# Performance work log

Measured on AMD Instinct MI355X. Metric: run time of the kernel, lower is better.

## Reference

```python
import jax, jax.numpy as jnp
import numpy as np

PI = np.float32(np.pi)
CNOT = jnp.array([[1,0,0,0],[0,1,0,0],[0,0,0,1],[0,0,1,0]], dtype=jnp.complex64)


def _u3(t, p, l):
    c, s = jnp.cos(t / 2), jnp.sin(t / 2)
    return jnp.stack([
        jnp.stack([c + 0j, -jnp.exp(1j * l) * s]),
        jnp.stack([jnp.exp(1j * p) * s, jnp.exp(1j * (p + l)) * c]),
    ]).astype(jnp.complex64)


def _ry(t):
    c, s = jnp.cos(t / 2), jnp.sin(t / 2)
    return jnp.stack([jnp.stack([c, -s]), jnp.stack([s, c])]).astype(jnp.complex64)


def _rz(t):
    z = jnp.zeros((), jnp.complex64)
    return jnp.stack([
        jnp.stack([jnp.exp(-1j * t / 2).astype(jnp.complex64), z]),
        jnp.stack([z, jnp.exp(1j * t / 2).astype(jnp.complex64)]),
    ]).astype(jnp.complex64)


def _apply1(psi, G, w):
    # psi: [N,2,2,2,2]; uniform single-qubit gate G [2,2] on wire w
    psi = jnp.moveaxis(psi, 1 + w, -1)
    psi = jnp.einsum('ij,nabcj->nabci', G, psi)
    return jnp.moveaxis(psi, -1, 1 + w)


def _apply1_batch(psi, G, w):
    # per-sample gate G [N,2,2]
    psi = jnp.moveaxis(psi, 1 + w, -1)
    psi = jnp.einsum('nij,nabcj->nabci', G, psi)
    return jnp.moveaxis(psi, -1, 1 + w)


def _apply2(psi, G, a, b):
    # two-qubit gate G [4,4] on wires (a,b)
    psi = jnp.moveaxis(psi, (1 + a, 1 + b), (-2, -1))
    psi = psi.reshape(psi.shape[:-2] + (4,))
    psi = jnp.einsum('ij,nabj->nabi', G, psi)
    psi = psi.reshape(psi.shape[:-1] + (2, 2))
    return jnp.moveaxis(psi, (-2, -1), (1 + a, 1 + b))


def _su4(psi, u3s, angs, a, b):
    # u3s: [4,3] = (w0, w1, w5, w6); angs: [3] = (w2, w3, w4)
    psi = _apply1(psi, _u3(u3s[0, 0], u3s[0, 1], u3s[0, 2]), a)
    psi = _apply1(psi, _u3(u3s[1, 0], u3s[1, 1], u3s[1, 2]), b)
    psi = _apply2(psi, CNOT, a, b)
    psi = _apply1(psi, _ry(angs[0]), a)
    psi = _apply1(psi, _rz(angs[1]), b)
    psi = _apply2(psi, CNOT, b, a)
    psi = _apply1(psi, _ry(angs[2]), a)
    psi = _apply2(psi, CNOT, a, b)
    psi = _apply1(psi, _u3(u3s[2, 0], u3s[2, 1], u3s[2, 2]), a)
    psi = _apply1(psi, _u3(u3s[3, 0], u3s[3, 1], u3s[3, 2]), b)
    return psi


def _circuit(angles, qw_u3, qw_ang):
    # angles: [N,4]; returns PauliZ expvals [N,4]
    N = angles.shape[0]
    psi = jnp.zeros((N, 2, 2, 2, 2), jnp.complex64).at[:, 0, 0, 0, 0].set(1.0)
    for w in range(4):  # AngleEmbedding: RY(angle) on each wire, per-sample
        c, s = jnp.cos(angles[:, w] / 2), jnp.sin(angles[:, w] / 2)
        G = jnp.stack([jnp.stack([c, -s], -1), jnp.stack([s, c], -1)], -2).astype(jnp.complex64)
        psi = _apply1_batch(psi, G, w)
    pairs = [(0, 1), (1, 2), (2, 3), (3, 0)]
    for layer in range(2):
        u3s = qw_u3[4 * layer:4 * layer + 4]
        angs = qw_ang[3 * layer:3 * layer + 3]
        for (a, b) in pairs:
            psi = _su4(psi, u3s, angs, a, b)
    p = psi.real ** 2 + psi.imag ** 2  # [N,2,2,2,2]
    z = jnp.array([1.0, -1.0], p.dtype)
    evs = [jnp.sum(p * z.reshape([1] + [2 if i == w else 1 for i in range(4)]), axis=(1, 2, 3, 4)) for w in range(4)]
    return jnp.stack(evs, -1)


def _conv(x, w, b):
    y = jax.lax.conv_general_dilated(x, w, (1, 1), 'SAME', dimension_numbers=('NCHW', 'OIHW', 'NCHW'))
    return y + b[None, :, None, None]


def _maxpool2(x):
    return jax.lax.reduce_window(x, -jnp.inf, jax.lax.max, (1, 1, 2, 2), (1, 1, 2, 2), 'VALID')


def setup_inputs() -> dict:
    key = jax.random.key(0)
    ks = jax.random.split(key, 20)
    n = jax.random.normal
    return {
        'x': n(ks[0], (1024, 3, 32, 32), jnp.float32),
        'conv1_w': n(ks[1], (64, 3, 3, 3), jnp.float32) * 0.1,
        'conv1_b': n(ks[2], (64,), jnp.float32) * 0.1,
        'conv2_w': n(ks[3], (16, 64, 3, 3), jnp.float32) * 0.05,
        'conv2_b': n(ks[4], (16,), jnp.float32) * 0.1,
        'conv3_w': n(ks[5], (4, 16, 3, 3), jnp.float32) * 0.1,
        'conv3_b': n(ks[6], (4,), jnp.float32) * 0.1,
        'qw_u3': jax.random.uniform(ks[7], (8, 3), jnp.float32, 0.0, 2 * np.pi),
        'qw_ang': jax.random.uniform(ks[8], (6,), jnp.float32, 0.0, 2 * np.pi),
        'fc1a_w': n(ks[9], (64, 256), jnp.float32) * 0.06,
        'fc1a_b': n(ks[10], (64,), jnp.float32) * 0.1,
        'fc1b_w': n(ks[11], (128, 64), jnp.float32) * 0.1,
        'fc1b_b': n(ks[12], (128,), jnp.float32) * 0.1,
        'fc2a_w': n(ks[13], (64, 128), jnp.float32) * 0.1,
        'fc2a_b': n(ks[14], (64,), jnp.float32) * 0.1,
        'fc2b_w': n(ks[15], (10, 64), jnp.float32) * 0.1,
        'fc2b_b': n(ks[16], (10,), jnp.float32) * 0.1,
    }


def reference(x, conv1_w, conv1_b, conv2_w, conv2_b, conv3_w, conv3_b,
              qw_u3, qw_ang, fc1a_w, fc1a_b, fc1b_w, fc1b_b,
              fc2a_w, fc2a_b, fc2b_w, fc2b_b):
    h = _maxpool2(jax.nn.relu(_conv(x, conv1_w, conv1_b)))      # [B,64,16,16]
    h = _maxpool2(jax.nn.relu(_conv(h, conv2_w, conv2_b)))      # [B,16,8,8]
    h = jax.nn.leaky_relu(_conv(h, conv3_w, conv3_b), 0.01)     # [B,4,8,8]
    B, C, H, W = h.shape
    # 1x1 patches in (h, w, c) order, matching torch unfold+permute
    patches = jnp.transpose(h, (0, 2, 3, 1)).reshape(B * H * W, C)
    ang = jax.nn.sigmoid(patches) * PI
    q = _circuit(ang, qw_u3, qw_ang)            # [B*64, 4]
    q = q.reshape(B, H * W * 4)                 # [B, 256]
    h1 = jax.nn.relu(q @ fc1a_w.T + fc1a_b)
    h1 = h1 @ fc1b_w.T + fc1b_b
    h2 = jax.nn.relu(h1 @ fc2a_w.T + fc2a_b)
    return h2 @ fc2b_w.T + fc2b_b               # [B, 10]
```

## Files before the change

kernel.cpp:

```cpp
#include <hip/hip_runtime.h>
#include <math.h>

#define PI_F 3.14159265358979323846f

typedef _Float16 half2_t __attribute__((ext_vector_type(2)));
typedef _Float16 f16x8 __attribute__((ext_vector_type(8)));
typedef float f32x4v __attribute__((ext_vector_type(4)));

__device__ __forceinline__ unsigned packh2(float lo, float hi) {
  unsigned short l = __builtin_bit_cast(unsigned short, (_Float16)lo);
  unsigned short h = __builtin_bit_cast(unsigned short, (_Float16)hi);
  return (unsigned)l | ((unsigned)h << 16);
}

__device__ __forceinline__ unsigned pk16(_Float16 a, _Float16 b) {
  unsigned short ua = __builtin_bit_cast(unsigned short, a);
  unsigned short ub = __builtin_bit_cast(unsigned short, b);
  return (unsigned)ua | ((unsigned)ub << 16);
}

struct c2 { float x, y; };
__device__ __forceinline__ c2 cmul(c2 a, c2 b){ return c2{a.x*b.x - a.y*b.y, a.x*b.y + a.y*b.x}; }
__device__ __forceinline__ c2 cadd(c2 a, c2 b){ return c2{a.x+b.x, a.y+b.y}; }

__device__ __forceinline__ void rot2(c2 &a, c2 &b, c2 g00, c2 g01, c2 g10, c2 g11) {
  c2 na = cadd(cmul(g00,a), cmul(g01,b));
  c2 nb = cadd(cmul(g10,a), cmul(g11,b));
  a = na; b = nb;
}

__device__ __forceinline__ void mk_u3(float th, float ph, float la,
                                      c2 &g00, c2 &g01, c2 &g10, c2 &g11) {
  float ch = cosf(0.5f*th), sh = sinf(0.5f*th);
  float cl = cosf(la), sl = sinf(la);
  float cp = cosf(ph), sp = sinf(ph);
  float cpl = cp*cl - sp*sl, spl = sp*cl + cp*sl;
  g00 = c2{ch, 0.f};
  g01 = c2{-cl*sh, -sl*sh};
  g10 = c2{cp*sh, sp*sh};
  g11 = c2{cpl*ch, spl*ch};
}

template<int MA, int MB>
__device__ __forceinline__ void apply2q(c2 psi[16], const c2 M[16]) {
#pragma unroll
  for (int r = 0; r < 16; ++r) {
    if (r & (MA | MB)) continue;
    c2 a = psi[r], b = psi[r|MB], c = psi[r|MA], d = psi[r|MA|MB];
    psi[r]        = cadd(cadd(cmul(M[0],a),  cmul(M[1],b)),  cadd(cmul(M[2],c),  cmul(M[3],d)));
    psi[r|MB]     = cadd(cadd(cmul(M[4],a),  cmul(M[5],b)),  cadd(cmul(M[6],c),  cmul(M[7],d)));
    psi[r|MA]     = cadd(cadd(cmul(M[8],a),  cmul(M[9],b)),  cadd(cmul(M[10],c), cmul(M[11],d)));
    psi[r|MA|MB]  = cadd(cadd(cmul(M[12],a), cmul(M[13],b)), cadd(cmul(M[14],c), cmul(M[15],d)));
  }
}

__global__ __launch_bounds__(256) void k_setup(const float* __restrict__ w1a, const float* __restrict__ w1b,
                                               const float* __restrict__ w2a, const float* __restrict__ w2b,
                                               const float* __restrict__ c2w,
                                               const float* __restrict__ c1w, const float* __restrict__ c1b,
                                               const float* __restrict__ qw_u3,
                                               const float* __restrict__ qw_ang,
                                               float* __restrict__ wt, float* __restrict__ A) {
  __shared__ c2 SU[2][16];
  __shared__ float Ur[16*17], Ui[16*17];
  int t = threadIdx.x;
  if (blockIdx.x == 167) {
    if (t < 8) {
      int L = t >> 2, col = t & 3;
      c2 s[4];
#pragma unroll
      for (int i = 0; i < 4; ++i) s[i] = c2{(i==col)?1.f:0.f, 0.f};
      const float* u = qw_u3 + 12*L;
      const float* g = qw_ang + 3*L;
      c2 g00,g01,g10,g11;
      mk_u3(u[0],u[1],u[2], g00,g01,g10,g11);
      rot2(s[0],s[2], g00,g01,g10,g11); rot2(s[1],s[3], g00,g01,g10,g11);
      mk_u3(u[3],u[4],u[5], g00,g01,g10,g11);
      rot2(s[0],s[1], g00,g01,g10,g11); rot2(s[2],s[3], g00,g01,g10,g11);
      { c2 tmp = s[2]; s[2] = s[3]; s[3] = tmp; }
      { float c = cosf(0.5f*g[0]), sn = sinf(0.5f*g[0]);
        c2 r00{c,0.f}, r01{-sn,0.f}, r10{sn,0.f}, r11{c,0.f};
        rot2(s[0],s[2], r00,r01,r10,r11); rot2(s[1],s[3], r00,r01,r10,r11); }
      { float c = cosf(0.5f*g[1]), sn = sinf(0.5f*g[1]);
        c2 e0{c,-sn}, e1{c,sn};
        s[0]=cmul(s[0],e0); s[1]=cmul(s[1],e1); s[2]=cmul(s[2],e0); s[3]=cmul(s[3],e1); }
      { c2 tmp = s[1]; s[1] = s[3]; s[3] = tmp; }
      { float c = cosf(0.5f*g[2]), sn = sinf(0.5f*g[2]);
        c2 r00{c,0.f}, r01{-sn,0.f}, r10{sn,0.f}, r11{c,0.f};
        rot2(s[0],s[2], r00,r01,r10,r11); rot2(s[1],s[3], r00,r01,r10,r11); }
      { c2 tmp = s[2]; s[2] = s[3]; s[3] = tmp; }
      mk_u3(u[6],u[7],u[8], g00,g01,g10,g11);
      rot2(s[0],s[2], g00,g01,g10,g11); rot2(s[1],s[3], g00,g01,g10,g11);
      mk_u3(u[9],u[10],u[11], g00,g01,g10,g11);
      rot2(s[0],s[1], g00,g01,g10,g11); rot2(s[2],s[3], g00,g01,g10,g11);
#pragma unroll
      for (int k = 0; k < 4; ++k) SU[L][k*4 + col] = s[k];
    }
    __syncthreads();
    if (t < 16) {
      c2 psi[16];
#pragma unroll
      for (int i = 0; i < 16; ++i) psi[i] = c2{(i==t)?1.f:0.f, 0.f};
#pragma unroll
      for (int l = 0; l < 2; ++l) {
        c2 M[16];
#pragma unroll
        for (int k = 0; k < 16; ++k) M[k] = SU[l][k];
        apply2q<8,4>(psi, M);
        apply2q<4,2>(psi, M);
        apply2q<2,1>(psi, M);
        apply2q<1,8>(psi, M);
      }
#pragma unroll
      for (int k = 0; k < 16; ++k) { Ur[k*17+t] = psi[k].x; Ui[k*17+t] = psi[k].y; }
    }
    __syncthreads();
    {
      int i = t >> 4, j = t & 15;
      float a0=0.f,a1=0.f,a2=0.f,a3=0.f;
#pragma unroll
      for (int k = 0; k < 16; ++k) {
        float pr = Ur[k*17+i]*Ur[k*17+j] + Ui[k*17+i]*Ui[k*17+j];
        a0 += ((k>>3)&1) ? -pr : pr;
        a1 += ((k>>2)&1) ? -pr : pr;
        a2 += ((k>>1)&1) ? -pr : pr;
        a3 += ( k     &1) ? -pr : pr;
      }
      A[0*256 + t] = a0; A[1*256 + t] = a1; A[2*256 + t] = a2; A[3*256 + t] = a3;
    }
    return;
  }
  int id = blockIdx.x*256 + t;
  if (id < 16384) { int j = id >> 6, o = id & 63;  wt[id] = w1a[o*256 + j]; return; }
  int id1 = id - 16384;
  if (id1 < 8192)  { int j = id1 >> 7, o = id1 & 127; wt[16384 + id1] = w1b[o*64 + j]; return; }
  int id2 = id1 - 8192;
  if (id2 < 8192)  { int j = id2 >> 6, o = id2 & 63;  wt[24576 + id2] = w2a[o*128 + j]; return; }
  int id3 = id2 - 8192;
  if (id3 < 640)   { int j = id3 / 10, o = id3 % 10;  wt[32768 + id3] = w2b[o*64 + j]; return; }
  int id4 = id3 - 640;
  if (id4 < 4608) {
    int s = id4 >> 8, rem = id4 & 255, l = rem >> 2, r = rem & 3;
    int tap = s >> 1, h = s & 1;
    int oc = l & 15, j = l >> 4;
    int icl = 16*h + 4*j + r;
    float lo = c2w[oc*576 + icl*9 + tap];
    float hi = c2w[oc*576 + (icl+32)*9 + tap];
    ((unsigned*)wt)[33408 + id4] = packh2(lo, hi);
    return;
  }
  int id5 = id4 - 4608;
  if (id5 < 1024) {
    int nt = id5 >> 8, rem = id5 & 255, l = rem >> 2, r = rem & 3;
    int oc = nt*16 + (l & 15), j = l >> 4;
    int k0 = 8*j + 2*r;
    float lo = (k0     < 27) ? c1w[oc*27 + k0]     : 0.f;
    float hi = (k0 + 1 < 27) ? c1w[oc*27 + k0 + 1] : 0.f;
    ((unsigned*)wt)[38016 + id5] = packh2(lo, hi);
  }
}

__global__ __launch_bounds__(512, 4) void k_conv12(
    const float* __restrict__ x,
    const uint4* __restrict__ B1g, const float* __restrict__ b1,
    const uint4* __restrict__ B2g, const float* __restrict__ b2,
    float* __restrict__ h2) {
  __shared__ _Float16 xs[3468];
  __shared__ unsigned hsp[11664];
  int b = blockIdx.x, t = threadIdx.x;
  int l = t & 63, w = t >> 6;
  int m = l & 15, j = l >> 4;
  uint4 Bf1[4];
#pragma unroll
  for (int nt = 0; nt < 4; ++nt) Bf1[nt] = B1g[nt*64 + l];
  int offs[8];
#pragma unroll
  for (int q = 0; q < 8; ++q) {
    int kk = 8*j + q;
    int kc = (kk < 27) ? kk : 0;
    int c = kc / 9, rem = kc - 9*c, wr = rem / 3, cc = rem - 3*wr;
    offs[q] = c*1156 + wr*34 + cc;
  }
  {
    unsigned* xz = (unsigned*)xs;
    for (int i = t; i < 1734; i += 512) xz[i] = 0u;
    uint4 z = make_uint4(0u,0u,0u,0u);
    uint4* hz = (uint4*)hsp;
    for (int i = t; i < 2916; i += 512) hz[i] = z;
  }
  __syncthreads();
  for (int i = t; i < 3072; i += 512) {
    int c = i >> 10, rem = i & 1023, gy = rem >> 5, gx = rem & 31;
    xs[c*1156 + (gy+1)*34 + gx + 1] = (_Float16)x[(size_t)b*3072 + i];
  }
  __syncthreads();
#pragma unroll
  for (int h = 0; h < 2; ++h) {
    f32x4v acc[2][2][4];
#pragma unroll
    for (int rr = 0; rr < 2; ++rr)
#pragma unroll
      for (int xh = 0; xh < 2; ++xh)
#pragma unroll
        for (int nt = 0; nt < 4; ++nt)
          acc[rr][xh][nt] = f32x4v{0.f, 0.f, 0.f, 0.f};
#pragma unroll
    for (int rr = 0; rr < 2; ++rr)
#pragma unroll
      for (int xh = 0; xh < 2; ++xh) {
        int base = (16*h + 2*w + rr)*34 + 16*xh + m;
        _Float16 v[8];
#pragma unroll
        for (int q = 0; q < 8; ++q) v[q] = xs[offs[q] + base];
        uint4 Au = make_uint4(pk16(v[0], v[1]), pk16(v[2], v[3]),
                              pk16(v[4], v[5]), pk16(v[6], v[7]));
        f16x8 Av = __builtin_bit_cast(f16x8, Au);
#pragma unroll
        for (int nt = 0; nt < 4; ++nt)
          acc[rr][xh][nt] = __builtin_amdgcn_mfma_f32_16x16x32_f16(
              Av, __builtin_bit_cast(f16x8, Bf1[nt]), acc[rr][xh][nt], 0, 0, 0);
      }
    {
      int pyg = 8*h + w;
#pragma unroll
      for (int ntp = 0; ntp < 2; ++ntp) {
        float bza = b1[ntp*16 + m];
        float bzb = b1[(ntp+2)*16 + m];
#pragma unroll
        for (int xh = 0; xh < 2; ++xh)
#pragma unroll
          for (int pv = 0; pv < 2; ++pv) {
            f32x4v aL0 = acc[0][xh][ntp],   aL1 = acc[1][xh][ntp];
            f32x4v aH0 = acc[0][xh][ntp+2], aH1 = acc[1][xh][ntp+2];
            float mlo = fmaxf(fmaxf(aL0[2*pv], aL0[2*pv+1]), fmaxf(aL1[2*pv], aL1[2*pv+1]));
            float mhi = fmaxf(fmaxf(aH0[2*pv], aH0[2*pv+1]), fmaxf(aH1[2*pv], aH1[2*pv+1]));
            int px = 8*xh + 2*j + pv;
            hsp[((pyg+1)*18 + px + 1)*36 + ntp*16 + m] =
                packh2(fmaxf(mlo + bza, 0.f), fmaxf(mhi + bzb, 0.f));
          }
      }
    }
  }
  __syncthreads();
  float bz2 = b2[m];
  f32x4v a2[2];
  a2[0] = f32x4v{bz2, bz2, bz2, bz2};
  a2[1] = f32x4v{bz2, bz2, bz2, bz2};
  uint4 bnx = B2g[l];
#pragma unroll
  for (int s = 0; s < 18; ++s) {
    f16x8 Bv = __builtin_bit_cast(f16x8, bnx);
    if (s < 17) bnx = B2g[(s+1)*64 + l];
    const int tap = s >> 1, hh = s & 1;
    const int dy = tap / 3, dx = tap % 3;
#pragma unroll
    for (int tt = 0; tt < 2; ++tt) {
      int y = 2*w + tt;
      f16x8 Av = __builtin_bit_cast(f16x8,
          *(const uint4*)(hsp + ((y+dy)*18 + m + dx)*36 + 16*hh + 4*j));
      a2[tt] = __builtin_amdgcn_mfma_f32_16x16x32_f16(Av, Bv, a2[tt], 0, 0, 0);
    }
  }
  float* outb = h2 + (size_t)b*1024 + m*64;
#pragma unroll
  for (int vp = 0; vp < 2; ++vp) {
    float mm = fmaxf(fmaxf(a2[0][2*vp], a2[0][2*vp+1]),
                     fmaxf(a2[1][2*vp], a2[1][2*vp+1]));
    outb[w*8 + 2*j + vp] = fmaxf(mm, 0.f);
  }
}

__global__ __launch_bounds__(256) void k_tail(const float* __restrict__ h2, const float* __restrict__ w,
                                              const float* __restrict__ bias, const float* __restrict__ Ag,
                                              const float* __restrict__ wt,
                                              const float* __restrict__ b1a, const float* __restrict__ b1b,
                                              const float* __restrict__ b2a, const float* __restrict__ b2b,
                                              float* __restrict__ out) {
  __shared__ float h3s[1600];
  __shared__ float As[1024];
  __shared__ float c3s[4][64];
  __shared__ float qs[256];
  __shared__ float red[256];
  __shared__ float h1s[64];
  __shared__ float hbv[128];
  __shared__ float h3v[64];
  int b = blockIdx.x, t = threadIdx.x;
#pragma unroll
  for (int k = 0; k < 4; ++k) As[k*256 + t] = Ag[k*256 + t];
  for (int i = t; i < 1600; i += 256) h3s[i] = 0.f;
  __syncthreads();
  {
    const float4* src = (const float4*)(h2 + (size_t)b*1024);
    float4 v = src[t];
    int e = 4*t;
    int ic = e >> 6, iy = (e >> 3) & 7, ix = e & 7;
    float* d = &h3s[ic*100 + (iy+1)*10 + ix + 1];
    d[0]=v.x; d[1]=v.y; d[2]=v.z; d[3]=v.w;
  }
  __syncthreads();
  {
    int oc = t >> 6, pos = t & 63;
    int y = pos >> 3, xo = pos & 7;
    float acc = bias[oc];
    const float* wp = w + oc*144;
    for (int ic = 0; ic < 16; ++ic) {
#pragma unroll
      for (int ky = 0; ky < 3; ++ky)
#pragma unroll
        for (int kx = 0; kx < 3; ++kx)
          acc = fmaf(wp[ic*9 + ky*3 + kx], h3s[ic*100 + (y+ky)*10 + (xo+kx)], acc);
    }
    c3s[oc][pos] = acc;
  }
  __syncthreads();
  {
    int p = t & 63, w4 = t >> 6;
    float v0[2], v1[2], v2[2], v3[2];
#pragma unroll
    for (int o = 0; o < 4; ++o) {
      float v = c3s[o][p];
      float lv = v > 0.f ? v : 0.01f*v;
      float sg = 1.f/(1.f + expf(-lv));
      float sv, cv;
      __sincosf(sg * (0.5f*PI_F), &sv, &cv);
      float* dst = (o==0)?v0:(o==1)?v1:(o==2)?v2:v3;
      dst[0] = cv; dst[1] = sv;
    }
    float pv[16];
#pragma unroll
    for (int i = 0; i < 16; ++i)
      pv[i] = v0[(i>>3)&1] * v1[(i>>2)&1] * v2[(i>>1)&1] * v3[i&1];
    const float4* Aw = (const float4*)(As + w4*256);
    float a = 0.f;
#pragma unroll
    for (int i = 0; i < 16; ++i) {
      float d = 0.f;
#pragma unroll
      for (int j4 = 0; j4 < 4; ++j4) {
        float4 av = Aw[i*4 + j4];
        d = fmaf(av.x, pv[j4*4+0], d);
        d = fmaf(av.y, pv[j4*4+1], d);
        d = fmaf(av.z, pv[j4*4+2], d);
        d = fmaf(av.w, pv[j4*4+3], d);
      }
      a = fmaf(pv[i], d, a);
    }
    qs[p*4 + w4] = a;
  }
  __syncthreads();
  const float* WT1a = wt;
  const float* WT1b = wt + 16384;
  const float* WT2a = wt + 24576;
  const float* WT2b = wt + 32768;
  {
    int o = t & 63, seg = t >> 6;
    float acc = 0.f;
    const float* wp = WT1a + seg*64*64 + o;
    const float* qp = qs + seg*64;
    for (int jj = 0; jj < 64; ++jj) acc = fmaf(wp[jj*64], qp[jj], acc);
    red[seg*64 + o] = acc;
  }
  __syncthreads();
  if (t < 64) {
    float s = red[t] + red[64+t] + red[128+t] + red[192+t] + b1a[t];
    h1s[t] = fmaxf(s, 0.f);
  }
  __syncthreads();
  if (t < 128) {
    float acc = b1b[t];
    for (int jj = 0; jj < 64; ++jj) acc = fmaf(WT1b[jj*128 + t], h1s[jj], acc);
    hbv[t] = acc;
  }
  __syncthreads();
  {
    int o = t & 63, seg = t >> 6;
    float acc = 0.f;
    const float* wp = WT2a + seg*32*64 + o;
    const float* hp = hbv + seg*32;
    for (int jj = 0; jj < 32; ++jj) acc = fmaf(wp[jj*64], hp[jj], acc);
    red[seg*64 + o] = acc;
  }
  __syncthreads();
  if (t < 64) {
    float s = red[t] + red[64+t] + red[128+t] + red[192+t] + b2a[t];
    h3v[t] = fmaxf(s, 0.f);
  }
  __syncthreads();
  if (t < 10) {
    float o = b2b[t];
    for (int jj = 0; jj < 64; ++jj) o = fmaf(WT2b[jj*10 + t], h3v[jj], o);
    out[(size_t)b*10 + t] = o;
  }
}

extern "C" void kernel_launch(void* const* d_in, const int* in_sizes, int n_in,
                              void* d_out, int out_size, void* d_ws, size_t ws_size,
                              hipStream_t stream) {
  const float* x       = (const float*)d_in[0];
  const float* conv1_w = (const float*)d_in[1];
  const float* conv1_b = (const float*)d_in[2];
  const float* conv2_w = (const float*)d_in[3];
  const float* conv2_b = (const float*)d_in[4];
  const float* conv3_w = (const float*)d_in[5];
  const float* conv3_b = (const float*)d_in[6];
  const float* qw_u3   = (const float*)d_in[7];
  const float* qw_ang  = (const float*)d_in[8];
  const float* fc1a_w  = (const float*)d_in[9];
  const float* fc1a_b  = (const float*)d_in[10];
  const float* fc1b_w  = (const float*)d_in[11];
  const float* fc1b_b  = (const float*)d_in[12];
  const float* fc2a_w  = (const float*)d_in[13];
  const float* fc2a_b  = (const float*)d_in[14];
  const float* fc2b_w  = (const float*)d_in[15];
  const float* fc2b_b  = (const float*)d_in[16];
  float* out = (float*)d_out;

  float* ws  = (float*)d_ws;
  float* A   = ws;
  float* WT  = ws + 1024;
  const uint4* BG  = (const uint4*)((const unsigned*)WT + 33408);
  const uint4* B1G = (const uint4*)((const unsigned*)WT + 38016);
  float* h2  = ws + 17083008;

  k_setup <<<168,  256, 0, stream>>>(fc1a_w, fc1b_w, fc2a_w, fc2b_w, conv2_w, conv1_w, conv1_b,
                                     qw_u3, qw_ang, WT, A);
  k_conv12<<<1024, 512, 0, stream>>>(x, B1G, conv1_b, BG, conv2_b, h2);
  k_tail  <<<1024, 256, 0, stream>>>(h2, conv3_w, conv3_b, A, WT,
                                     fc1a_b, fc1b_b, fc2a_b, fc2b_b, out);
}
```

Measured before the change: 45.87 us.

## Process two images per tail block and prefetch conv1 input before zeroing

The tail kernel now handles two batch images per block, halving the grid. This amortizes the shared-memory load of the quantum matrix and the per-block weight traffic, and uses idle threads in the small FC stages. Separately, conv12 issues its global input loads into registers before the shared-memory zeroing and barrier, so load latency overlaps with that setup. The cost is more shared memory and more serial work per tail block, with only half as many blocks to spread across CUs.

```diff
diff --git a/kernel.cpp b/kernel.cpp
--- a/kernel.cpp
+++ b/kernel.cpp
@@ -170,6 +170,9 @@
   int b = blockIdx.x, t = threadIdx.x;
   int l = t & 63, w = t >> 6;
   int m = l & 15, j = l >> 4;
+  float xr[6];
+#pragma unroll
+  for (int k = 0; k < 6; ++k) xr[k] = x[(size_t)b*3072 + t + k*512];
   uint4 Bf1[4];
 #pragma unroll
   for (int nt = 0; nt < 4; ++nt) Bf1[nt] = B1g[nt*64 + l];
@@ -189,9 +192,11 @@
     for (int i = t; i < 2916; i += 512) hz[i] = z;
   }
   __syncthreads();
-  for (int i = t; i < 3072; i += 512) {
+#pragma unroll
+  for (int k = 0; k < 6; ++k) {
+    int i = t + k*512;
     int c = i >> 10, rem = i & 1023, gy = rem >> 5, gx = rem & 31;
-    xs[c*1156 + (gy+1)*34 + gx + 1] = (_Float16)x[(size_t)b*3072 + i];
+    xs[c*1156 + (gy+1)*34 + gx + 1] = (_Float16)xr[k];
   }
   __syncthreads();
 #pragma unroll
@@ -276,76 +281,84 @@
                                               const float* __restrict__ b1a, const float* __restrict__ b1b,
                                               const float* __restrict__ b2a, const float* __restrict__ b2b,
                                               float* __restrict__ out) {
-  __shared__ float h3s[1600];
+  __shared__ float h3s[2][1600];
   __shared__ float As[1024];
-  __shared__ float c3s[4][64];
-  __shared__ float qs[256];
-  __shared__ float red[256];
-  __shared__ float h1s[64];
-  __shared__ float hbv[128];
-  __shared__ float h3v[64];
-  int b = blockIdx.x, t = threadIdx.x;
+  __shared__ float c3s[2][4][64];
+  __shared__ float qs[2][256];
+  __shared__ float red[2][256];
+  __shared__ float h1s[2][64];
+  __shared__ float hbv[2][128];
+  __shared__ float h3v[2][64];
+  int blk = blockIdx.x, t = threadIdx.x;
+  int b0 = blk*2;
 #pragma unroll
   for (int k = 0; k < 4; ++k) As[k*256 + t] = Ag[k*256 + t];
-  for (int i = t; i < 1600; i += 256) h3s[i] = 0.f;
-  __syncthreads();
-  {
-    const float4* src = (const float4*)(h2 + (size_t)b*1024);
+  for (int i = t; i < 3200; i += 256) h3s[0][i] = 0.f;
+  __syncthreads();
+#pragma unroll
+  for (int im = 0; im < 2; ++im) {
+    const float4* src = (const float4*)(h2 + (size_t)(b0+im)*1024);
     float4 v = src[t];
     int e = 4*t;
     int ic = e >> 6, iy = (e >> 3) & 7, ix = e & 7;
-    float* d = &h3s[ic*100 + (iy+1)*10 + ix + 1];
+    float* d = &h3s[im][ic*100 + (iy+1)*10 + ix + 1];
     d[0]=v.x; d[1]=v.y; d[2]=v.z; d[3]=v.w;
   }
   __syncthreads();
   {
     int oc = t >> 6, pos = t & 63;
     int y = pos >> 3, xo = pos & 7;
-    float acc = bias[oc];
     const float* wp = w + oc*144;
-    for (int ic = 0; ic < 16; ++ic) {
-#pragma unroll
-      for (int ky = 0; ky < 3; ++ky)
-#pragma unroll
-        for (int kx = 0; kx < 3; ++kx)
-          acc = fmaf(wp[ic*9 + ky*3 + kx], h3s[ic*100 + (y+ky)*10 + (xo+kx)], acc);
-    }
-    c3s[oc][pos] = acc;
+#pragma unroll
+    for (int im = 0; im < 2; ++im) {
+      float acc = bias[oc];
+      for (int ic = 0; ic < 16; ++ic) {
+#pragma unroll
+        for (int ky = 0; ky < 3; ++ky)
+#pragma unroll
+          for (int kx = 0; kx < 3; ++kx)
+            acc = fmaf(wp[ic*9 + ky*3 + kx], h3s[im][ic*100 + (y+ky)*10 + (xo+kx)], acc);
+      }
+      c3s[im][oc][pos] = acc;
+    }
   }
   __syncthreads();
   {
     int p = t & 63, w4 = t >> 6;
-    float v0[2], v1[2], v2[2], v3[2];
-#pragma unroll
-    for (int o = 0; o < 4; ++o) {
-      float v = c3s[o][p];
-      float lv = v > 0.f ? v : 0.01f*v;
-      float sg = 1.f/(1.f + expf(-lv));
-      float sv, cv;
-      __sincosf(sg * (0.5f*PI_F), &sv, &cv);
-      float* dst = (o==0)?v0:(o==1)?v1:(o==2)?v2:v3;
-      dst[0] = cv; dst[1] = sv;
-    }
-    float pv[16];
-#pragma unroll
-    for (int i = 0; i < 16; ++i)
-      pv[i] = v0[(i>>3)&1] * v1[(i>>2)&1] * v2[(i>>1)&1] * v3[i&1];
-    const float4* Aw = (const float4*)(As + w4*256);
-    float a = 0.f;
-#pragma unroll
-    for (int i = 0; i < 16; ++i) {
-      float d = 0.f;
-#pragma unroll
-      for (int j4 = 0; j4 < 4; ++j4) {
-        float4 av = Aw[i*4 + j4];
-        d = fmaf(av.x, pv[j4*4+0], d);
-        d = fmaf(av.y, pv[j4*4+1], d);
-        d = fmaf(av.z, pv[j4*4+2], d);
-        d = fmaf(av.w, pv[j4*4+3], d);
-      }
-      a = fmaf(pv[i], d, a);
-    }
-    qs[p*4 + w4] = a;
+#pragma unroll
+    for (int im = 0; im < 2; ++im) {
+      float v0[2], v1[2], v2[2], v3[2];
+#pragma unroll
+      for (int o = 0; o < 4; ++o) {
+        float v = c3s[im][o][p];
+        float lv = v > 0.f ? v : 0.01f*v;
+        float sg = 1.f/(1.f + expf(-lv));
+        float sv, cv;
+        __sincosf(sg * (0.5f*PI_F), &sv, &cv);
+        float* dst = (o==0)?v0:(o==1)?v1:(o==2)?v2:v3;
+        dst[0] = cv; dst[1] = sv;
+      }
+      float pv[16];
+#pragma unroll
+      for (int i = 0; i < 16; ++i)
+        pv[i] = v0[(i>>3)&1] * v1[(i>>2)&1] * v2[(i>>1)&1] * v3[i&1];
+      const float4* Aw = (const float4*)(As + w4*256);
+      float a = 0.f;
+#pragma unroll
+      for (int i = 0; i < 16; ++i) {
+        float d = 0.f;
+#pragma unroll
+        for (int j4 = 0; j4 < 4; ++j4) {
+          float4 av = Aw[i*4 + j4];
+          d = fmaf(av.x, pv[j4*4+0], d);
+          d = fmaf(av.y, pv[j4*4+1], d);
+          d = fmaf(av.z, pv[j4*4+2], d);
+          d = fmaf(av.w, pv[j4*4+3], d);
+        }
+        a = fmaf(pv[i], d, a);
+      }
+      qs[im][p*4 + w4] = a;
+    }
   }
   __syncthreads();
   const float* WT1a = wt;
@@ -354,42 +367,54 @@
   const float* WT2b = wt + 32768;
   {
     int o = t & 63, seg = t >> 6;
-    float acc = 0.f;
     const float* wp = WT1a + seg*64*64 + o;
-    const float* qp = qs + seg*64;
-    for (int jj = 0; jj < 64; ++jj) acc = fmaf(wp[jj*64], qp[jj], acc);
-    red[seg*64 + o] = acc;
-  }
-  __syncthreads();
-  if (t < 64) {
-    float s = red[t] + red[64+t] + red[128+t] + red[192+t] + b1a[t];
-    h1s[t] = fmaxf(s, 0.f);
+#pragma unroll
+    for (int im = 0; im < 2; ++im) {
+      float acc = 0.f;
+      const float* qp = qs[im] + seg*64;
+      for (int jj = 0; jj < 64; ++jj) acc = fmaf(wp[jj*64], qp[jj], acc);
+      red[im][seg*64 + o] = acc;
+    }
   }
   __syncthreads();
   if (t < 128) {
-    float acc = b1b[t];
-    for (int jj = 0; jj < 64; ++jj) acc = fmaf(WT1b[jj*128 + t], h1s[jj], acc);
-    hbv[t] = acc;
+    int im = t >> 6, o = t & 63;
+    float s = red[im][o] + red[im][64+o] + red[im][128+o] + red[im][192+o] + b1a[o];
+    h1s[im][o] = fmaxf(s, 0.f);
+  }
+  __syncthreads();
+  {
+    int im = t >> 7, o = t & 127;
+    float acc = b1b[o];
+    for (int jj = 0; jj < 64; ++jj) acc = fmaf(WT1b[jj*128 + o], h1s[im][jj], acc);
+    hbv[im][o] = acc;
   }
   __syncthreads();
   {
     int o = t & 63, seg = t >> 6;
-    float acc = 0.f;
     const float* wp = WT2a + seg*32*64 + o;
-    const float* hp = hbv + seg*32;
-    for (int jj = 0; jj < 32; ++jj) acc = fmaf(wp[jj*64], hp[jj], acc);
-    red[seg*64 + o] = acc;
-  }
-  __syncthreads();
-  if (t < 64) {
-    float s = red[t] + red[64+t] + red[128+t] + red[192+t] + b2a[t];
-    h3v[t] = fmaxf(s, 0.f);
-  }
-  __syncthreads();
-  if (t < 10) {
-    float o = b2b[t];
-    for (int jj = 0; jj < 64; ++jj) o = fmaf(WT2b[jj*10 + t], h3v[jj], o);
-    out[(size_t)b*10 + t] = o;
+#pragma unroll
+    for (int im = 0; im < 2; ++im) {
+      float acc = 0.f;
+      const float* hp = hbv[im] + seg*32;
+      for (int jj = 0; jj < 32; ++jj) acc = fmaf(wp[jj*64], hp[jj], acc);
+      red[im][seg*64 + o] = acc;
+    }
+  }
+  __syncthreads();
+  if (t < 128) {
+    int im = t >> 6, o = t & 63;
+    float s = red[im][o] + red[im][64+o] + red[im][128+o] + red[im][192+o] + b2a[o];
+    h3v[im][o] = fmaxf(s, 0.f);
+  }
+  __syncthreads();
+  {
+    int im = t >> 7, o = t & 127;
+    if (o < 10) {
+      float acc = b2b[o];
+      for (int jj = 0; jj < 64; ++jj) acc = fmaf(WT2b[jj*10 + o], h3v[im][jj], acc);
+      out[(size_t)(b0+im)*10 + o] = acc;
+    }
   }
 }
 
@@ -425,6 +450,6 @@
   k_setup <<<168,  256, 0, stream>>>(fc1a_w, fc1b_w, fc2a_w, fc2b_w, conv2_w, conv1_w, conv1_b,
                                      qw_u3, qw_ang, WT, A);
   k_conv12<<<1024, 512, 0, stream>>>(x, B1G, conv1_b, BG, conv2_b, h2);
-  k_tail  <<<1024, 256, 0, stream>>>(h2, conv3_w, conv3_b, A, WT,
+  k_tail  <<<512,  256, 0, stream>>>(h2, conv3_w, conv3_b, A, WT,
                                      fc1a_b, fc1b_b, fc2a_b, fc2b_b, out);
 }
```

Measured after the change: 51.27 us. 1.12x slower.
